# Kernel optimization log

Hardware: AMD Instinct MI355X
Metric: run time of the kernel (lower is better)

## Reference

```python
import jax, jax.numpy as jnp
import numpy as np

B = 131072
NUM_MODS = 6
NUM_PREDS = 30
CLS_TH = 2.0
CLS_IGNORE = 0.2
MGN = 0.2
CLS_COEF = 1.0
REG_COEF = 1.0


def setup_inputs() -> dict:
    key = jax.random.key(0)
    k1, k2, k3 = jax.random.split(key, 3)
    reg = jax.random.normal(k1, (B, NUM_MODS, NUM_PREDS, 2), jnp.float32)
    cls = jax.random.normal(k2, (B, NUM_MODS), jnp.float32)
    gt_preds = jax.random.normal(k3, (B, NUM_PREDS, 2), jnp.float32)
    has_preds = jnp.ones((B, NUM_PREDS), dtype=bool)
    return {"reg": reg, "cls": cls, "gt_preds": gt_preds, "has_preds": has_preds}


def _loss(reg, cls, gt, has):
    # ---------------- PredLoss (LaneGCN cls + reg loss) ----------------
    hasf = has.astype(jnp.float32)
    last = hasf + 0.1 * jnp.arange(NUM_PREDS, dtype=jnp.float32) / float(NUM_PREDS)
    last_idcs = jnp.argmax(last, axis=1)                      # [B]
    max_last = jnp.max(last, axis=1)
    valid = max_last > 1.0                                    # [B] rows kept by `mask`

    # distance of each mode's last-valid point to gt last-valid point
    reg_last = jnp.take_along_axis(reg, last_idcs[:, None, None, None], axis=2)[:, :, 0, :]  # [B,6,2]
    gt_last = jnp.take_along_axis(gt, last_idcs[:, None, None], axis=1)[:, 0, :]             # [B,2]
    dist = jnp.sqrt(((reg_last - gt_last[:, None, :]) ** 2).sum(-1))                          # [B,6]

    min_idcs = jnp.argmin(dist, axis=1)                       # [B]
    min_dist = jnp.min(dist, axis=1)

    cls_min = jnp.take_along_axis(cls, min_idcs[:, None], axis=1)  # [B,1]
    mgn = cls_min - cls                                            # [B,6]
    m01 = (min_dist < CLS_TH)[:, None] & ((dist - min_dist[:, None]) > CLS_IGNORE) & valid[:, None]
    cls_mask = m01 & (mgn < MGN)
    num_cls = cls_mask.sum()
    cls_loss = CLS_COEF * (MGN * num_cls.astype(jnp.float32) - jnp.where(cls_mask, mgn, 0.0).sum())

    # SmoothL1 (beta=1, reduction='sum') over best mode, masked by has & valid
    reg_best = jnp.take_along_axis(reg, min_idcs[:, None, None, None], axis=1)[:, 0]  # [B,30,2]
    diff = reg_best - gt
    ad = jnp.abs(diff)
    sl1 = jnp.where(ad < 1.0, 0.5 * diff * diff, ad - 0.5)
    w = (has & valid[:, None]).astype(jnp.float32)[..., None]  # [B,30,1]
    reg_loss = REG_COEF * (sl1 * w).sum()
    num_reg = (has & valid[:, None]).sum()

    loss = cls_loss / (num_cls.astype(jnp.float32) + 1e-10) + reg_loss / (num_reg.astype(jnp.float32) + 1e-10)

    # ---------------- heading (vectorized over scenes) ----------------
    gx, gy = gt[..., 0], gt[..., 1]                           # [B,30]
    fwd = jnp.arctan2(gy[:, 2:] - gy[:, 1:-1], gx[:, 2:] - gx[:, 1:-1])   # [B,28]
    bwd = jnp.arctan2(gy[:, 1:-1] - gy[:, :-2], gx[:, 1:-1] - gx[:, :-2]) # [B,28]
    head_tmp = jnp.rad2deg(fwd) + jnp.rad2deg(bwd)                         # [B,28]
    mid = jnp.where((fwd == 0.0) | (bwd == 0.0), head_tmp, head_tmp / 2.0)
    head0 = jnp.rad2deg(jnp.arctan2(gy[:, 1] - gy[:, 0], gx[:, 1] - gx[:, 0]))
    headL = jnp.rad2deg(jnp.arctan2(gy[:, -1] - gy[:, -2], gx[:, -1] - gx[:, -2]))
    head = jnp.concatenate([head0[:, None], mid, headL[:, None]], axis=1)  # [B,30]
    moving = jnp.sqrt(((gt[:, 0, :] - gt[:, -1, :]) ** 2).sum(-1)) > 2.0
    head = jnp.where(moving[:, None], head, 0.0)

    # ---------------- rotated dist_error (per-timestep 2x2 rotation) ----------------
    de0 = jnp.abs(gt[:, None, :, :] - reg)                    # [B,6,30,2] L1Loss(reduction='none')
    theta = jnp.deg2rad(-head)                                # [B,30]
    c = jnp.cos(theta)[:, None, :]                            # [B,1,30]
    s = jnp.sin(theta)[:, None, :]
    dx, dy = de0[..., 0], de0[..., 1]                         # [B,6,30]
    rx = c * dx - s * dy
    ry = s * dx + c * dy
    de = jnp.abs(jnp.stack([rx, ry], axis=-1))                # [B,6,30,2]

    top1 = jnp.argmax(cls, axis=1)                            # [B]
    de_top = jnp.take_along_axis(de, top1[:, None, None, None], axis=1)[:, 0]  # [B,30,2]

    ade6_x = de[..., 0].sum(); ade6_y = de[..., 1].sum()
    fde6_x = de[:, :, -1, 0].sum(); fde6_y = de[:, :, -1, 1].sum()
    ade1_x = de_top[..., 0].sum(); ade1_y = de_top[..., 1].sum()
    fde1_x = de_top[:, -1, 0].sum(); fde1_y = de_top[:, -1, 1].sum()

    Bn = de.shape[0]
    counts = jnp.array([
        NUM_MODS * Bn * NUM_PREDS,  # ade6_num
        NUM_MODS * Bn,              # fde6_num
        Bn * NUM_PREDS,             # ade1_num
        Bn,                         # fde1_num
    ], dtype=jnp.float32)

    return jnp.stack([
        loss, cls_loss, num_cls.astype(jnp.float32), reg_loss, num_reg.astype(jnp.float32),
        ade6_x, ade6_y, fde6_x, fde6_y, counts[0], counts[1],
        ade1_x, ade1_y, fde1_x, fde1_y, counts[2], counts[3],
    ])


def reference(reg, cls, gt_preds, has_preds):
    return _loss(reg, cls, gt_preds, has_preds)
```

## Files before the change

kernel.cpp:

```cpp
#include <hip/hip_runtime.h>
#include <math.h>

#define NROWS 131072
#define NMODS 6
#define NPREDS 30
#define RPG 4
#define NGROUPS (NROWS / RPG)
#define NBLK 2048
#define NWAVES (NBLK * 4)

#define ACC_SLOT(ws, i) ((float*)((char*)(ws) + (size_t)(i) * 256))

#define LGKM_WAIT() do { \
    __builtin_amdgcn_wave_barrier(); \
    __builtin_amdgcn_s_waitcnt(0xC07F); \
    __builtin_amdgcn_wave_barrier(); \
} while (0)

__device__ __forceinline__ float wave_reduce(float v) {
    v += __shfl_xor(v, 32);
    v += __shfl_xor(v, 16);
    v += __shfl_xor(v, 8);
    v += __shfl_xor(v, 4);
    v += __shfl_xor(v, 2);
    v += __shfl_xor(v, 1);
    return v;
}

__global__ __launch_bounds__(256) void loss_wave(
    const float* __restrict__ reg,
    const float* __restrict__ cls,
    const float* __restrict__ gt,
    const int* __restrict__ has,
    void* __restrict__ ws)
{
    const int tid   = threadIdx.x;
    const int lane  = tid & 63;
    const int wid   = tid >> 6;
    const int gwave = blockIdx.x * 4 + wid;

    __shared__ float4 s_gt[4][RPG * 15];
    __shared__ float4 s_ct[4][RPG * 15];
    __shared__ float  s_red[4][12];

    const int row = lane / 15;
    const int q   = lane - row * 15;

    float acc[12];
    #pragma unroll
    for (int i = 0; i < 12; ++i) acc[i] = 0.f;

    for (int g = gwave; g < NGROUPS; g += NWAVES) {
        const int rb = g * RPG;

        float4 gv = make_float4(0.f, 0.f, 0.f, 0.f);
        int2   hv = make_int2(0, 0);
        if (lane < 60) {
            gv = ((const float4*)gt)[(size_t)rb * 15 + lane];
            hv = ((const int2*)has)[(size_t)rb * 15 + lane];
        }
        const float4* reg4 = (const float4*)reg + (size_t)rb * 90;
        float4 rv[6];
        #pragma unroll
        for (int i = 0; i < 5; ++i) rv[i] = reg4[lane + 64 * i];
        if (lane < 40) rv[5] = reg4[lane + 320];

        unsigned long long bx = __ballot(lane < 60 && hv.x != 0);
        unsigned long long by = __ballot(lane < 60 && hv.y != 0);

        unsigned ex = 0u, ey = 0u;
        int last = NPREDS - 1;
        bool valid = false;
        float2 rl[NMODS];
        float2 cc[3];
        if (lane < RPG) {
            ex = (unsigned)((bx >> (15 * lane)) & 0x7FFFull);
            ey = (unsigned)((by >> (15 * lane)) & 0x7FFFull);
            int le = ex ? 2 * (31 - __builtin_clz(ex)) : -1;
            int lo = ey ? 2 * (31 - __builtin_clz(ey)) + 1 : -1;
            last = (le > lo) ? le : lo;
            if (last < 0) last = NPREDS - 1;
            valid = ((ex & ~1u) | ey) != 0u;

            const float2* rr = (const float2*)reg + (size_t)(rb + lane) * 180;
            #pragma unroll
            for (int m = 0; m < NMODS; ++m) rl[m] = rr[m * NPREDS + last];
            const float2* cp = (const float2*)cls + (size_t)(rb + lane) * 3;
            #pragma unroll
            for (int i = 0; i < 3; ++i) cc[i] = cp[i];
        }

        float e_dx = gv.z - gv.x, e_dy = gv.w - gv.y;
        float e_inv = rsqrtf(fmaf(e_dx, e_dx, e_dy * e_dy));
        float uex = e_dx * e_inv, uey = e_dy * e_inv;

        float nx = __shfl(gv.x, lane + 1);
        float ny = __shfl(gv.y, lane + 1);
        float o_dx = nx - gv.z, o_dy = ny - gv.w;
        float o_inv = rsqrtf(fmaf(o_dx, o_dx, o_dy * o_dy));
        float uox = o_dx * o_inv, uoy = o_dy * o_inv;

        float upx = __shfl(uox, lane - 1);
        float upy = __shfl(uoy, lane - 1);

        const int base = row * 15;
        float g0x  = __shfl(gv.x, base),      g0y  = __shfl(gv.y, base);
        float g29x = __shfl(gv.z, base + 14), g29y = __shfl(gv.w, base + 14);
        float mdx = g0x - g29x, mdy = g0y - g29y;
        const bool moving = fmaf(mdx, mdx, mdy * mdy) > 4.0f;

        float sx0 = uex + upx, sy0 = uey + upy;
        float dx0 = uey - upy, dy0 = upx - uex;
        float na0 = fmaf(sx0, sx0, sy0 * sy0);
        float nb0 = fmaf(dx0, dx0, dy0 * dy0);
        bool ua0 = na0 >= nb0;
        float wx0 = ua0 ? sx0 : dx0, wy0 = ua0 ? sy0 : dy0;
        float wi0 = rsqrtf(ua0 ? na0 : nb0);
        float c0 = wx0 * wi0, s0 = -(wy0 * wi0);
        if (q == 0) { c0 = uex; s0 = -uey; }

        float sx1 = uox + uex, sy1 = uoy + uey;
        float dx1 = uoy - uey, dy1 = uex - uox;
        float na1 = fmaf(sx1, sx1, sy1 * sy1);
        float nb1 = fmaf(dx1, dx1, dy1 * dy1);
        bool ua1 = na1 >= nb1;
        float wx1 = ua1 ? sx1 : dx1, wy1 = ua1 ? sy1 : dy1;
        float wi1 = rsqrtf(ua1 ? na1 : nb1);
        float c1 = wx1 * wi1, s1 = -(wy1 * wi1);
        if (q == 14) { c1 = uex; s1 = -uey; }

        if (!moving) { c0 = 1.f; s0 = 0.f; c1 = 1.f; s1 = 0.f; }

        if (lane < 60) {
            s_gt[wid][lane] = gv;
            s_ct[wid][lane] = make_float4(c0, s0, c1, s1);
        }
        LGKM_WAIT();

        unsigned metaval = 0u;
        if (lane < RPG) {
            float4 gq = s_gt[wid][lane * 15 + (last >> 1)];
            float glx = (last & 1) ? gq.z : gq.x;
            float gly = (last & 1) ? gq.w : gq.y;

            float dists[NMODS];
            #pragma unroll
            for (int m = 0; m < NMODS; ++m) {
                float ax = rl[m].x - glx, ay = rl[m].y - gly;
                dists[m] = sqrtf(ax * ax + ay * ay);
            }
            float mind = dists[0]; int mini = 0;
            #pragma unroll
            for (int m = 1; m < NMODS; ++m)
                if (dists[m] < mind) { mind = dists[m]; mini = m; }

            float cv[NMODS];
            #pragma unroll
            for (int i = 0; i < 3; ++i) { cv[2*i] = cc[i].x; cv[2*i+1] = cc[i].y; }
            float clsmin = cv[0];
            #pragma unroll
            for (int m = 1; m < NMODS; ++m) clsmin = (m == mini) ? cv[m] : clsmin;

            if (valid && (mind < 2.0f)) {
                #pragma unroll
                for (int m = 0; m < NMODS; ++m) {
                    float mgn = clsmin - cv[m];
                    if (((dists[m] - mind) > 0.2f) && (mgn < 0.2f)) {
                        acc[10] += 1.0f;
                        acc[9]  += mgn;
                    }
                }
            }
            float bc = cv[0]; int top1 = 0;
            #pragma unroll
            for (int m = 1; m < NMODS; ++m)
                if (cv[m] > bc) { bc = cv[m]; top1 = m; }

            if (valid)
                acc[11] += (float)(__builtin_popcount(ex) + __builtin_popcount(ey));

            metaval = (unsigned)mini | ((unsigned)top1 << 4) | (valid ? 256u : 0u);
        }

        #pragma unroll
        for (int i = 0; i < 6; ++i) {
            int k = lane + 64 * i;
            bool act = (i < 5) || (lane < 40);
            int kk = act ? k : 0;
            int rw  = kk / 90;
            int rem = kk - rw * 90;
            int m   = rem / 15;
            int qq  = rem - 15 * m;

            unsigned mv  = (unsigned)__shfl((int)metaval, rw);
            unsigned exr = (unsigned)((bx >> (15 * rw)) & 0x7FFFull);
            unsigned eyr = (unsigned)((by >> (15 * rw)) & 0x7FFFull);
            float4 gp = s_gt[wid][rw * 15 + qq];
            float4 sp = s_ct[wid][rw * 15 + qq];
            float4 v  = rv[i];

            unsigned mini = mv & 15u, top1 = (mv >> 4) & 15u;
            bool vld    = (mv & 256u) != 0u;
            bool isTop  = ((unsigned)m == top1);
            bool isBest = ((unsigned)m == mini) && vld;

            if (act) {
                {
                    float dx = fabsf(gp.x - v.x), dy = fabsf(gp.y - v.y);
                    float ax = fabsf(sp.x * dx - sp.y * dy);
                    float ay = fabsf(sp.y * dx + sp.x * dy);
                    acc[0] += ax; acc[1] += ay;
                    if (isTop) { acc[4] += ax; acc[5] += ay; }
                    if (isBest && ((exr >> qq) & 1u)) {
                        float e0 = v.x - gp.x, e1 = v.y - gp.y;
                        float q0 = fabsf(e0), q1 = fabsf(e1);
                        acc[8] += (q0 < 1.f) ? (0.5f * e0 * e0) : (q0 - 0.5f);
                        acc[8] += (q1 < 1.f) ? (0.5f * e1 * e1) : (q1 - 0.5f);
                    }
                }
                {
                    float dx = fabsf(gp.z - v.z), dy = fabsf(gp.w - v.w);
                    float ax = fabsf(sp.z * dx - sp.w * dy);
                    float ay = fabsf(sp.w * dx + sp.z * dy);
                    acc[0] += ax; acc[1] += ay;
                    if (isTop) { acc[4] += ax; acc[5] += ay; }
                    if (qq == 14) {
                        acc[2] += ax; acc[3] += ay;
                        if (isTop) { acc[6] += ax; acc[7] += ay; }
                    }
                    if (isBest && ((eyr >> qq) & 1u)) {
                        float e0 = v.z - gp.z, e1 = v.w - gp.w;
                        float q0 = fabsf(e0), q1 = fabsf(e1);
                        acc[8] += (q0 < 1.f) ? (0.5f * e0 * e0) : (q0 - 0.5f);
                        acc[8] += (q1 < 1.f) ? (0.5f * e1 * e1) : (q1 - 0.5f);
                    }
                }
            }
        }
        __builtin_amdgcn_wave_barrier();
    }

    #pragma unroll
    for (int i = 0; i < 12; ++i) acc[i] = wave_reduce(acc[i]);

    if (lane == 0) {
        #pragma unroll
        for (int i = 0; i < 12; ++i) s_red[wid][i] = acc[i];
    }
    __syncthreads();
    if (tid < 12) {
        float s = s_red[0][tid] + s_red[1][tid] + s_red[2][tid] + s_red[3][tid];
        atomicAdd(ACC_SLOT(ws, tid), s);
    }
}

__global__ void finalize(void* ws, float* __restrict__ out) {
    if (threadIdx.x == 0) {
        float nc = *ACC_SLOT(ws, 10), nr = *ACC_SLOT(ws, 11);
        float cls_loss = 0.2f * nc - *ACC_SLOT(ws, 9);
        float reg_loss = *ACC_SLOT(ws, 8);
        float loss = cls_loss / (nc + 1e-10f) + reg_loss / (nr + 1e-10f);
        out[0]  = loss;
        out[1]  = cls_loss;
        out[2]  = nc;
        out[3]  = reg_loss;
        out[4]  = nr;
        out[5]  = *ACC_SLOT(ws, 0);
        out[6]  = *ACC_SLOT(ws, 1);
        out[7]  = *ACC_SLOT(ws, 2);
        out[8]  = *ACC_SLOT(ws, 3);
        out[9]  = 23592960.0f;
        out[10] = 786432.0f;
        out[11] = *ACC_SLOT(ws, 4);
        out[12] = *ACC_SLOT(ws, 5);
        out[13] = *ACC_SLOT(ws, 6);
        out[14] = *ACC_SLOT(ws, 7);
        out[15] = 3932160.0f;
        out[16] = 131072.0f;
    }
}

extern "C" void kernel_launch(void* const* d_in, const int* in_sizes, int n_in,
                              void* d_out, int out_size, void* d_ws, size_t ws_size,
                              hipStream_t stream) {
    const float* reg = (const float*)d_in[0];
    const float* cls = (const float*)d_in[1];
    const float* gt  = (const float*)d_in[2];
    const int*   has = (const int*)d_in[3];
    float* out = (float*)d_out;

    hipMemsetAsync(d_ws, 0, 4096, stream);
    loss_wave<<<NBLK, 256, 0, stream>>>(reg, cls, gt, has, d_ws);
    finalize<<<1, 64, 0, stream>>>(d_ws, out);
}
```

Measured before the change: 303.2 us.

## Fuse finalize into main kernel and restructure per-element loop via shared scatter

```diff
diff --git a/kernel.cpp b/kernel.cpp
--- a/kernel.cpp
+++ b/kernel.cpp
@@ -10,6 +10,7 @@
 #define NWAVES (NBLK * 4)
 
 #define ACC_SLOT(ws, i) ((float*)((char*)(ws) + (size_t)(i) * 256))
+#define TICKET(ws) ((unsigned*)((char*)(ws) + 3072))
 
 #define LGKM_WAIT() do { \
     __builtin_amdgcn_wave_barrier(); \
@@ -32,19 +33,35 @@
     const float* __restrict__ cls,
     const float* __restrict__ gt,
     const int* __restrict__ has,
-    void* __restrict__ ws)
+    void* __restrict__ ws,
+    float* __restrict__ out)
 {
     const int tid   = threadIdx.x;
     const int lane  = tid & 63;
     const int wid   = tid >> 6;
     const int gwave = blockIdx.x * 4 + wid;
 
-    __shared__ float4 s_gt[4][RPG * 15];
-    __shared__ float4 s_ct[4][RPG * 15];
+    __shared__ float4 s_tile[4][216];
     __shared__ float  s_red[4][12];
+    __shared__ int    s_last;
 
     const int row = lane / 15;
     const int q   = lane - row * 15;
+
+    int   rwv[6];  int mmv[6];  int idxv[6];  float f14v[6];
+    #pragma unroll
+    for (int i = 0; i < 6; ++i) {
+        int k = lane + 64 * i;
+        bool act = (i < 5) || (lane < 40);
+        int kk = act ? k : 0;
+        int rw  = kk / 90;
+        int rem = kk - rw * 90;
+        int mm  = rem / 15;
+        int qq  = rem - 15 * mm;
+        rwv[i] = rw; mmv[i] = mm; idxv[i] = rw * 15 + qq;
+        f14v[i] = (qq == 14) ? 1.f : 0.f;
+    }
+    const int dumidx = 180 + (lane & 31);
 
     float acc[12];
     #pragma unroll
@@ -65,6 +82,13 @@
         for (int i = 0; i < 5; ++i) rv[i] = reg4[lane + 64 * i];
         if (lane < 40) rv[5] = reg4[lane + 320];
 
+        float2 cc[3];
+        if (lane < RPG) {
+            const float2* cp = (const float2*)cls + (size_t)(rb + lane) * 3;
+            #pragma unroll
+            for (int i = 0; i < 3; ++i) cc[i] = cp[i];
+        }
+
         unsigned long long bx = __ballot(lane < 60 && hv.x != 0);
         unsigned long long by = __ballot(lane < 60 && hv.y != 0);
 
@@ -72,7 +96,6 @@
         int last = NPREDS - 1;
         bool valid = false;
         float2 rl[NMODS];
-        float2 cc[3];
         if (lane < RPG) {
             ex = (unsigned)((bx >> (15 * lane)) & 0x7FFFull);
             ey = (unsigned)((by >> (15 * lane)) & 0x7FFFull);
@@ -85,9 +108,6 @@
             const float2* rr = (const float2*)reg + (size_t)(rb + lane) * 180;
             #pragma unroll
             for (int m = 0; m < NMODS; ++m) rl[m] = rr[m * NPREDS + last];
-            const float2* cp = (const float2*)cls + (size_t)(rb + lane) * 3;
-            #pragma unroll
-            for (int i = 0; i < 3; ++i) cc[i] = cp[i];
         }
 
         float e_dx = gv.z - gv.x, e_dy = gv.w - gv.y;
@@ -132,27 +152,27 @@
         if (!moving) { c0 = 1.f; s0 = 0.f; c1 = 1.f; s1 = 0.f; }
 
         if (lane < 60) {
-            s_gt[wid][lane] = gv;
-            s_ct[wid][lane] = make_float4(c0, s0, c1, s1);
+            s_tile[wid][lane]      = gv;
+            s_tile[wid][60 + lane] = make_float4(c0, s0, c1, s1);
         }
         LGKM_WAIT();
 
         unsigned metaval = 0u;
         if (lane < RPG) {
-            float4 gq = s_gt[wid][lane * 15 + (last >> 1)];
+            float4 gq = s_tile[wid][lane * 15 + (last >> 1)];
             float glx = (last & 1) ? gq.z : gq.x;
             float gly = (last & 1) ? gq.w : gq.y;
 
-            float dists[NMODS];
+            float d2s[NMODS];
             #pragma unroll
             for (int m = 0; m < NMODS; ++m) {
                 float ax = rl[m].x - glx, ay = rl[m].y - gly;
-                dists[m] = sqrtf(ax * ax + ay * ay);
+                d2s[m] = fmaf(ax, ax, ay * ay);
             }
-            float mind = dists[0]; int mini = 0;
+            float mind2 = d2s[0]; int mini = 0;
             #pragma unroll
             for (int m = 1; m < NMODS; ++m)
-                if (dists[m] < mind) { mind = dists[m]; mini = m; }
+                if (d2s[m] < mind2) { mind2 = d2s[m]; mini = m; }
 
             float cv[NMODS];
             #pragma unroll
@@ -161,11 +181,14 @@
             #pragma unroll
             for (int m = 1; m < NMODS; ++m) clsmin = (m == mini) ? cv[m] : clsmin;
 
-            if (valid && (mind < 2.0f)) {
+            if (valid && (mind2 < 4.0f)) {
+                float mind = sqrtf(mind2);
+                float t = mind + 0.2f;
+                float thr = t * t;
                 #pragma unroll
                 for (int m = 0; m < NMODS; ++m) {
                     float mgn = clsmin - cv[m];
-                    if (((dists[m] - mind) > 0.2f) && (mgn < 0.2f)) {
+                    if ((d2s[m] > thr) && (mgn < 0.2f)) {
                         acc[10] += 1.0f;
                         acc[9]  += mgn;
                     }
@@ -184,59 +207,60 @@
 
         #pragma unroll
         for (int i = 0; i < 6; ++i) {
-            int k = lane + 64 * i;
-            bool act = (i < 5) || (lane < 40);
-            int kk = act ? k : 0;
-            int rw  = kk / 90;
-            int rem = kk - rw * 90;
-            int m   = rem / 15;
-            int qq  = rem - 15 * m;
-
-            unsigned mv  = (unsigned)__shfl((int)metaval, rw);
-            unsigned exr = (unsigned)((bx >> (15 * rw)) & 0x7FFFull);
-            unsigned eyr = (unsigned)((by >> (15 * rw)) & 0x7FFFull);
-            float4 gp = s_gt[wid][rw * 15 + qq];
-            float4 sp = s_ct[wid][rw * 15 + qq];
-            float4 v  = rv[i];
-
-            unsigned mini = mv & 15u, top1 = (mv >> 4) & 15u;
-            bool vld    = (mv & 256u) != 0u;
-            bool isTop  = ((unsigned)m == top1);
-            bool isBest = ((unsigned)m == mini) && vld;
-
+            const bool act = (i < 5) || (lane < 40);
+            unsigned mvb = (unsigned)__shfl((int)metaval, rwv[i]);
+            unsigned mini = mvb & 15u, top1 = (mvb >> 4) & 15u;
+            float tf = ((unsigned)mmv[i] == top1) ? 1.f : 0.f;
+            bool bestm = ((unsigned)mmv[i] == mini);
             if (act) {
-                {
-                    float dx = fabsf(gp.x - v.x), dy = fabsf(gp.y - v.y);
-                    float ax = fabsf(sp.x * dx - sp.y * dy);
-                    float ay = fabsf(sp.y * dx + sp.x * dy);
-                    acc[0] += ax; acc[1] += ay;
-                    if (isTop) { acc[4] += ax; acc[5] += ay; }
-                    if (isBest && ((exr >> qq) & 1u)) {
-                        float e0 = v.x - gp.x, e1 = v.y - gp.y;
-                        float q0 = fabsf(e0), q1 = fabsf(e1);
-                        acc[8] += (q0 < 1.f) ? (0.5f * e0 * e0) : (q0 - 0.5f);
-                        acc[8] += (q1 < 1.f) ? (0.5f * e1 * e1) : (q1 - 0.5f);
-                    }
-                }
-                {
-                    float dx = fabsf(gp.z - v.z), dy = fabsf(gp.w - v.w);
-                    float ax = fabsf(sp.z * dx - sp.w * dy);
-                    float ay = fabsf(sp.w * dx + sp.z * dy);
-                    acc[0] += ax; acc[1] += ay;
-                    if (isTop) { acc[4] += ax; acc[5] += ay; }
-                    if (qq == 14) {
-                        acc[2] += ax; acc[3] += ay;
-                        if (isTop) { acc[6] += ax; acc[7] += ay; }
-                    }
-                    if (isBest && ((eyr >> qq) & 1u)) {
-                        float e0 = v.z - gp.z, e1 = v.w - gp.w;
-                        float q0 = fabsf(e0), q1 = fabsf(e1);
-                        acc[8] += (q0 < 1.f) ? (0.5f * e0 * e0) : (q0 - 0.5f);
-                        acc[8] += (q1 < 1.f) ? (0.5f * e1 * e1) : (q1 - 0.5f);
-                    }
-                }
+                float4* gpp = &s_tile[wid][idxv[i]];
+                float4 gp = gpp[0];
+                float4 sp = gpp[60];
+                float4 v  = rv[i];
+
+                float d0x = gp.x - v.x, d0y = gp.y - v.y;
+                float ax0 = fabsf(fmaf(sp.x, fabsf(d0x), -(sp.y * fabsf(d0y))));
+                float ay0 = fabsf(fmaf(sp.y, fabsf(d0x),   sp.x * fabsf(d0y)));
+                acc[0] += ax0; acc[1] += ay0;
+                acc[4] = fmaf(tf, ax0, acc[4]); acc[5] = fmaf(tf, ay0, acc[5]);
+
+                float d1x = gp.z - v.z, d1y = gp.w - v.w;
+                float ax1 = fabsf(fmaf(sp.z, fabsf(d1x), -(sp.w * fabsf(d1y))));
+                float ay1 = fabsf(fmaf(sp.w, fabsf(d1x),   sp.z * fabsf(d1y)));
+                acc[0] += ax1; acc[1] += ay1;
+                acc[4] = fmaf(tf, ax1, acc[4]); acc[5] = fmaf(tf, ay1, acc[5]);
+
+                float f14 = f14v[i];
+                acc[2] = fmaf(f14, ax1, acc[2]); acc[3] = fmaf(f14, ay1, acc[3]);
+                float tf14 = tf * f14;
+                acc[6] = fmaf(tf14, ax1, acc[6]); acc[7] = fmaf(tf14, ay1, acc[7]);
+
+                float4* dmy = &s_tile[wid][dumidx - 120];
+                float4* wa  = bestm ? gpp : dmy;
+                wa[120] = v;
             }
         }
+
+        LGKM_WAIT();
+
+        if (lane < 60) {
+            unsigned mvr = (unsigned)__shfl((int)metaval, row);
+            float4 bb = s_tile[wid][120 + lane];
+            bool vld = (mvr & 256u) != 0u;
+            unsigned bitx = (unsigned)(bx >> lane) & 1u;
+            unsigned bity = (unsigned)(by >> lane) & 1u;
+            float g0 = (vld && bitx) ? 1.f : 0.f;
+            float g1 = (vld && bity) ? 1.f : 0.f;
+            float e0x = bb.x - gv.x, e0y = bb.y - gv.y;
+            float e1x = bb.z - gv.z, e1y = bb.w - gv.w;
+            float sl0 = ((fabsf(e0x) < 1.f) ? (0.5f * e0x * e0x) : (fabsf(e0x) - 0.5f))
+                      + ((fabsf(e0y) < 1.f) ? (0.5f * e0y * e0y) : (fabsf(e0y) - 0.5f));
+            float sl1 = ((fabsf(e1x) < 1.f) ? (0.5f * e1x * e1x) : (fabsf(e1x) - 0.5f))
+                      + ((fabsf(e1y) < 1.f) ? (0.5f * e1y * e1y) : (fabsf(e1y) - 0.5f));
+            acc[8] = fmaf(g0, sl0, acc[8]);
+            acc[8] = fmaf(g1, sl1, acc[8]);
+        }
+
         __builtin_amdgcn_wave_barrier();
     }
 
@@ -252,31 +276,39 @@
         float s = s_red[0][tid] + s_red[1][tid] + s_red[2][tid] + s_red[3][tid];
         atomicAdd(ACC_SLOT(ws, tid), s);
     }
-}
-
-__global__ void finalize(void* ws, float* __restrict__ out) {
-    if (threadIdx.x == 0) {
-        float nc = *ACC_SLOT(ws, 10), nr = *ACC_SLOT(ws, 11);
-        float cls_loss = 0.2f * nc - *ACC_SLOT(ws, 9);
-        float reg_loss = *ACC_SLOT(ws, 8);
-        float loss = cls_loss / (nc + 1e-10f) + reg_loss / (nr + 1e-10f);
-        out[0]  = loss;
-        out[1]  = cls_loss;
-        out[2]  = nc;
-        out[3]  = reg_loss;
-        out[4]  = nr;
-        out[5]  = *ACC_SLOT(ws, 0);
-        out[6]  = *ACC_SLOT(ws, 1);
-        out[7]  = *ACC_SLOT(ws, 2);
-        out[8]  = *ACC_SLOT(ws, 3);
-        out[9]  = 23592960.0f;
-        out[10] = 786432.0f;
-        out[11] = *ACC_SLOT(ws, 4);
-        out[12] = *ACC_SLOT(ws, 5);
-        out[13] = *ACC_SLOT(ws, 6);
-        out[14] = *ACC_SLOT(ws, 7);
-        out[15] = 3932160.0f;
-        out[16] = 131072.0f;
+    __syncthreads();
+
+    if (tid == 0) {
+        __threadfence();
+        s_last = (atomicAdd(TICKET(ws), 1u) == (unsigned)(NBLK - 1)) ? 1 : 0;
+    }
+    __syncthreads();
+    if (s_last) {
+        if (tid < 12)
+            s_red[0][tid] = atomicAdd(ACC_SLOT(ws, tid), 0.0f);
+        __syncthreads();
+        if (tid == 0) {
+            float nc = s_red[0][10], nr = s_red[0][11];
+            float cls_loss = 0.2f * nc - s_red[0][9];
+            float reg_loss = s_red[0][8];
+            out[0]  = cls_loss / (nc + 1e-10f) + reg_loss / (nr + 1e-10f);
+            out[1]  = cls_loss;
+            out[2]  = nc;
+            out[3]  = reg_loss;
+            out[4]  = nr;
+            out[5]  = s_red[0][0];
+            out[6]  = s_red[0][1];
+            out[7]  = s_red[0][2];
+            out[8]  = s_red[0][3];
+            out[9]  = 23592960.0f;
+            out[10] = 786432.0f;
+            out[11] = s_red[0][4];
+            out[12] = s_red[0][5];
+            out[13] = s_red[0][6];
+            out[14] = s_red[0][7];
+            out[15] = 3932160.0f;
+            out[16] = 131072.0f;
+        }
     }
 }
 
@@ -290,6 +322,5 @@
     float* out = (float*)d_out;
 
     hipMemsetAsync(d_ws, 0, 4096, stream);
-    loss_wave<<<NBLK, 256, 0, stream>>>(reg, cls, gt, has, d_ws);
-    finalize<<<1, 64, 0, stream>>>(d_ws, out);
+    loss_wave<<<NBLK, 256, 0, stream>>>(reg, cls, gt, has, d_ws, out);
 }
```

Measured after the change: 385.3 us. +27.1%, slower.

## Software-pipeline per-group head loads across iterations with double-buffered state

Applied to the files above, without the earlier changes.

```diff
diff --git a/kernel.cpp b/kernel.cpp
--- a/kernel.cpp
+++ b/kernel.cpp
@@ -25,6 +25,232 @@
     v += __shfl_xor(v, 2);
     v += __shfl_xor(v, 1);
     return v;
+}
+
+struct GState {
+    float4 gv;
+    int2   hv;
+    float2 cc0, cc1, cc2;
+    float2 rl0, rl1, rl2, rl3, rl4, rl5;
+    unsigned long long bx, by;
+    unsigned ex, ey;
+    int last;
+    int validf;
+};
+
+__device__ __forceinline__ void issue_head(
+    int g, int lane,
+    const float* __restrict__ gt, const int* __restrict__ has,
+    const float* __restrict__ cls, GState& s)
+{
+    const int rb = g * RPG;
+    s.gv = make_float4(0.f, 0.f, 0.f, 0.f);
+    s.hv = make_int2(0, 0);
+    if (lane < 60) {
+        s.gv = ((const float4*)gt)[(size_t)rb * 15 + lane];
+        s.hv = ((const int2*)has)[(size_t)rb * 15 + lane];
+    }
+    if (lane < RPG) {
+        const float2* cp = (const float2*)cls + (size_t)(rb + lane) * 3;
+        s.cc0 = cp[0]; s.cc1 = cp[1]; s.cc2 = cp[2];
+    }
+}
+
+__device__ __forceinline__ void resolve_mask(
+    int g, int lane, const float* __restrict__ reg, GState& s)
+{
+    s.bx = __ballot(lane < 60 && s.hv.x != 0);
+    s.by = __ballot(lane < 60 && s.hv.y != 0);
+    s.ex = 0u; s.ey = 0u; s.last = NPREDS - 1; s.validf = 0;
+    if (lane < RPG) {
+        s.ex = (unsigned)((s.bx >> (15 * lane)) & 0x7FFFull);
+        s.ey = (unsigned)((s.by >> (15 * lane)) & 0x7FFFull);
+        int le = s.ex ? 2 * (31 - __builtin_clz(s.ex)) : -1;
+        int lo = s.ey ? 2 * (31 - __builtin_clz(s.ey)) + 1 : -1;
+        int last = (le > lo) ? le : lo;
+        if (last < 0) last = NPREDS - 1;
+        s.last = last;
+        s.validf = (((s.ex & ~1u) | s.ey) != 0u) ? 1 : 0;
+        const float2* rr = (const float2*)reg + (size_t)(g * RPG + lane) * 180;
+        s.rl0 = rr[0 * NPREDS + last];
+        s.rl1 = rr[1 * NPREDS + last];
+        s.rl2 = rr[2 * NPREDS + last];
+        s.rl3 = rr[3 * NPREDS + last];
+        s.rl4 = rr[4 * NPREDS + last];
+        s.rl5 = rr[5 * NPREDS + last];
+    }
+}
+
+__device__ __forceinline__ void body(
+    int g, bool pf, GState& cur, GState& nxt,
+    const float* __restrict__ reg, const float* __restrict__ cls,
+    const float* __restrict__ gt, const int* __restrict__ has,
+    int lane, int row, int q,
+    float4* __restrict__ sgt, float4* __restrict__ sct,
+    float acc[12])
+{
+    const int rb = g * RPG;
+
+    if (pf) issue_head(g + NWAVES, lane, gt, has, cls, nxt);
+
+    const float4* reg4 = (const float4*)reg + (size_t)rb * 90;
+    float4 rv[6];
+    #pragma unroll
+    for (int i = 0; i < 5; ++i) rv[i] = reg4[lane + 64 * i];
+    if (lane < 40) rv[5] = reg4[lane + 320];
+
+    const float4 gv = cur.gv;
+
+    float e_dx = gv.z - gv.x, e_dy = gv.w - gv.y;
+    float e_inv = rsqrtf(fmaf(e_dx, e_dx, e_dy * e_dy));
+    float uex = e_dx * e_inv, uey = e_dy * e_inv;
+
+    float nx = __shfl(gv.x, lane + 1);
+    float ny = __shfl(gv.y, lane + 1);
+    float o_dx = nx - gv.z, o_dy = ny - gv.w;
+    float o_inv = rsqrtf(fmaf(o_dx, o_dx, o_dy * o_dy));
+    float uox = o_dx * o_inv, uoy = o_dy * o_inv;
+
+    float upx = __shfl(uox, lane - 1);
+    float upy = __shfl(uoy, lane - 1);
+
+    const int base = row * 15;
+    float g0x  = __shfl(gv.x, base),      g0y  = __shfl(gv.y, base);
+    float g29x = __shfl(gv.z, base + 14), g29y = __shfl(gv.w, base + 14);
+    float mdx = g0x - g29x, mdy = g0y - g29y;
+    const bool moving = fmaf(mdx, mdx, mdy * mdy) > 4.0f;
+
+    float sx0 = uex + upx, sy0 = uey + upy;
+    float dx0 = uey - upy, dy0 = upx - uex;
+    float na0 = fmaf(sx0, sx0, sy0 * sy0);
+    float nb0 = fmaf(dx0, dx0, dy0 * dy0);
+    bool ua0 = na0 >= nb0;
+    float wx0 = ua0 ? sx0 : dx0, wy0 = ua0 ? sy0 : dy0;
+    float wi0 = rsqrtf(ua0 ? na0 : nb0);
+    float c0 = wx0 * wi0, s0 = -(wy0 * wi0);
+    if (q == 0) { c0 = uex; s0 = -uey; }
+
+    float sx1 = uox + uex, sy1 = uoy + uey;
+    float dx1 = uoy - uey, dy1 = uex - uox;
+    float na1 = fmaf(sx1, sx1, sy1 * sy1);
+    float nb1 = fmaf(dx1, dx1, dy1 * dy1);
+    bool ua1 = na1 >= nb1;
+    float wx1 = ua1 ? sx1 : dx1, wy1 = ua1 ? sy1 : dy1;
+    float wi1 = rsqrtf(ua1 ? na1 : nb1);
+    float c1 = wx1 * wi1, s1 = -(wy1 * wi1);
+    if (q == 14) { c1 = uex; s1 = -uey; }
+
+    if (!moving) { c0 = 1.f; s0 = 0.f; c1 = 1.f; s1 = 0.f; }
+
+    if (lane < 60) {
+        sgt[lane] = gv;
+        sct[lane] = make_float4(c0, s0, c1, s1);
+    }
+    LGKM_WAIT();
+
+    unsigned metaval = 0u;
+    if (lane < RPG) {
+        float4 gq = sgt[lane * 15 + (cur.last >> 1)];
+        float glx = (cur.last & 1) ? gq.z : gq.x;
+        float gly = (cur.last & 1) ? gq.w : gq.y;
+
+        float2 rl[NMODS] = { cur.rl0, cur.rl1, cur.rl2, cur.rl3, cur.rl4, cur.rl5 };
+        float dists[NMODS];
+        #pragma unroll
+        for (int m = 0; m < NMODS; ++m) {
+            float ax = rl[m].x - glx, ay = rl[m].y - gly;
+            dists[m] = sqrtf(ax * ax + ay * ay);
+        }
+        float mind = dists[0]; int mini = 0;
+        #pragma unroll
+        for (int m = 1; m < NMODS; ++m)
+            if (dists[m] < mind) { mind = dists[m]; mini = m; }
+
+        float cv[NMODS] = { cur.cc0.x, cur.cc0.y, cur.cc1.x, cur.cc1.y, cur.cc2.x, cur.cc2.y };
+        float clsmin = cv[0];
+        #pragma unroll
+        for (int m = 1; m < NMODS; ++m) clsmin = (m == mini) ? cv[m] : clsmin;
+
+        if (cur.validf && (mind < 2.0f)) {
+            #pragma unroll
+            for (int m = 0; m < NMODS; ++m) {
+                float mgn = clsmin - cv[m];
+                if (((dists[m] - mind) > 0.2f) && (mgn < 0.2f)) {
+                    acc[10] += 1.0f;
+                    acc[9]  += mgn;
+                }
+            }
+        }
+        float bc = cv[0]; int top1 = 0;
+        #pragma unroll
+        for (int m = 1; m < NMODS; ++m)
+            if (cv[m] > bc) { bc = cv[m]; top1 = m; }
+
+        if (cur.validf)
+            acc[11] += (float)(__builtin_popcount(cur.ex) + __builtin_popcount(cur.ey));
+
+        metaval = (unsigned)mini | ((unsigned)top1 << 4) | (cur.validf ? 256u : 0u);
+    }
+
+    #pragma unroll
+    for (int i = 0; i < 6; ++i) {
+        int k = lane + 64 * i;
+        bool act = (i < 5) || (lane < 40);
+        int kk = act ? k : 0;
+        int rw  = kk / 90;
+        int rem = kk - rw * 90;
+        int m   = rem / 15;
+        int qq  = rem - 15 * m;
+
+        unsigned mv  = (unsigned)__shfl((int)metaval, rw);
+        unsigned exr = (unsigned)((cur.bx >> (15 * rw)) & 0x7FFFull);
+        unsigned eyr = (unsigned)((cur.by >> (15 * rw)) & 0x7FFFull);
+        float4 gp = sgt[rw * 15 + qq];
+        float4 sp = sct[rw * 15 + qq];
+        float4 v  = rv[i];
+
+        unsigned mini = mv & 15u, top1 = (mv >> 4) & 15u;
+        bool vld    = (mv & 256u) != 0u;
+        bool isTop  = ((unsigned)m == top1);
+        bool isBest = ((unsigned)m == mini) && vld;
+
+        if (act) {
+            {
+                float dx = fabsf(gp.x - v.x), dy = fabsf(gp.y - v.y);
+                float ax = fabsf(sp.x * dx - sp.y * dy);
+                float ay = fabsf(sp.y * dx + sp.x * dy);
+                acc[0] += ax; acc[1] += ay;
+                if (isTop) { acc[4] += ax; acc[5] += ay; }
+                if (isBest && ((exr >> qq) & 1u)) {
+                    float e0 = v.x - gp.x, e1 = v.y - gp.y;
+                    float q0 = fabsf(e0), q1 = fabsf(e1);
+                    acc[8] += (q0 < 1.f) ? (0.5f * e0 * e0) : (q0 - 0.5f);
+                    acc[8] += (q1 < 1.f) ? (0.5f * e1 * e1) : (q1 - 0.5f);
+                }
+            }
+            {
+                float dx = fabsf(gp.z - v.z), dy = fabsf(gp.w - v.w);
+                float ax = fabsf(sp.z * dx - sp.w * dy);
+                float ay = fabsf(sp.w * dx + sp.z * dy);
+                acc[0] += ax; acc[1] += ay;
+                if (isTop) { acc[4] += ax; acc[5] += ay; }
+                if (qq == 14) {
+                    acc[2] += ax; acc[3] += ay;
+                    if (isTop) { acc[6] += ax; acc[7] += ay; }
+                }
+                if (isBest && ((eyr >> qq) & 1u)) {
+                    float e0 = v.z - gp.z, e1 = v.w - gp.w;
+                    float q0 = fabsf(e0), q1 = fabsf(e1);
+                    acc[8] += (q0 < 1.f) ? (0.5f * e0 * e0) : (q0 - 0.5f);
+                    acc[8] += (q1 < 1.f) ? (0.5f * e1 * e1) : (q1 - 0.5f);
+                }
+            }
+        }
+    }
+
+    if (pf) resolve_mask(g + NWAVES, lane, reg, nxt);
+
+    __builtin_amdgcn_wave_barrier();
 }
 
 __global__ __launch_bounds__(256) void loss_wave(
@@ -46,198 +272,23 @@
     const int row = lane / 15;
     const int q   = lane - row * 15;
 
+    float4* sgt = &s_gt[wid][0];
+    float4* sct = &s_ct[wid][0];
+
     float acc[12];
     #pragma unroll
     for (int i = 0; i < 12; ++i) acc[i] = 0.f;
 
-    for (int g = gwave; g < NGROUPS; g += NWAVES) {
-        const int rb = g * RPG;
-
-        float4 gv = make_float4(0.f, 0.f, 0.f, 0.f);
-        int2   hv = make_int2(0, 0);
-        if (lane < 60) {
-            gv = ((const float4*)gt)[(size_t)rb * 15 + lane];
-            hv = ((const int2*)has)[(size_t)rb * 15 + lane];
-        }
-        const float4* reg4 = (const float4*)reg + (size_t)rb * 90;
-        float4 rv[6];
-        #pragma unroll
-        for (int i = 0; i < 5; ++i) rv[i] = reg4[lane + 64 * i];
-        if (lane < 40) rv[5] = reg4[lane + 320];
-
-        unsigned long long bx = __ballot(lane < 60 && hv.x != 0);
-        unsigned long long by = __ballot(lane < 60 && hv.y != 0);
-
-        unsigned ex = 0u, ey = 0u;
-        int last = NPREDS - 1;
-        bool valid = false;
-        float2 rl[NMODS];
-        float2 cc[3];
-        if (lane < RPG) {
-            ex = (unsigned)((bx >> (15 * lane)) & 0x7FFFull);
-            ey = (unsigned)((by >> (15 * lane)) & 0x7FFFull);
-            int le = ex ? 2 * (31 - __builtin_clz(ex)) : -1;
-            int lo = ey ? 2 * (31 - __builtin_clz(ey)) + 1 : -1;
-            last = (le > lo) ? le : lo;
-            if (last < 0) last = NPREDS - 1;
-            valid = ((ex & ~1u) | ey) != 0u;
-
-            const float2* rr = (const float2*)reg + (size_t)(rb + lane) * 180;
-            #pragma unroll
-            for (int m = 0; m < NMODS; ++m) rl[m] = rr[m * NPREDS + last];
-            const float2* cp = (const float2*)cls + (size_t)(rb + lane) * 3;
-            #pragma unroll
-            for (int i = 0; i < 3; ++i) cc[i] = cp[i];
-        }
-
-        float e_dx = gv.z - gv.x, e_dy = gv.w - gv.y;
-        float e_inv = rsqrtf(fmaf(e_dx, e_dx, e_dy * e_dy));
-        float uex = e_dx * e_inv, uey = e_dy * e_inv;
-
-        float nx = __shfl(gv.x, lane + 1);
-        float ny = __shfl(gv.y, lane + 1);
-        float o_dx = nx - gv.z, o_dy = ny - gv.w;
-        float o_inv = rsqrtf(fmaf(o_dx, o_dx, o_dy * o_dy));
-        float uox = o_dx * o_inv, uoy = o_dy * o_inv;
-
-        float upx = __shfl(uox, lane - 1);
-        float upy = __shfl(uoy, lane - 1);
-
-        const int base = row * 15;
-        float g0x  = __shfl(gv.x, base),      g0y  = __shfl(gv.y, base);
-        float g29x = __shfl(gv.z, base + 14), g29y = __shfl(gv.w, base + 14);
-        float mdx = g0x - g29x, mdy = g0y - g29y;
-        const bool moving = fmaf(mdx, mdx, mdy * mdy) > 4.0f;
-
-        float sx0 = uex + upx, sy0 = uey + upy;
-        float dx0 = uey - upy, dy0 = upx - uex;
-        float na0 = fmaf(sx0, sx0, sy0 * sy0);
-        float nb0 = fmaf(dx0, dx0, dy0 * dy0);
-        bool ua0 = na0 >= nb0;
-        float wx0 = ua0 ? sx0 : dx0, wy0 = ua0 ? sy0 : dy0;
-        float wi0 = rsqrtf(ua0 ? na0 : nb0);
-        float c0 = wx0 * wi0, s0 = -(wy0 * wi0);
-        if (q == 0) { c0 = uex; s0 = -uey; }
-
-        float sx1 = uox + uex, sy1 = uoy + uey;
-        float dx1 = uoy - uey, dy1 = uex - uox;
-        float na1 = fmaf(sx1, sx1, sy1 * sy1);
-        float nb1 = fmaf(dx1, dx1, dy1 * dy1);
-        bool ua1 = na1 >= nb1;
-        float wx1 = ua1 ? sx1 : dx1, wy1 = ua1 ? sy1 : dy1;
-        float wi1 = rsqrtf(ua1 ? na1 : nb1);
-        float c1 = wx1 * wi1, s1 = -(wy1 * wi1);
-        if (q == 14) { c1 = uex; s1 = -uey; }
-
-        if (!moving) { c0 = 1.f; s0 = 0.f; c1 = 1.f; s1 = 0.f; }
-
-        if (lane < 60) {
-            s_gt[wid][lane] = gv;
-            s_ct[wid][lane] = make_float4(c0, s0, c1, s1);
-        }
-        LGKM_WAIT();
-
-        unsigned metaval = 0u;
-        if (lane < RPG) {
-            float4 gq = s_gt[wid][lane * 15 + (last >> 1)];
-            float glx = (last & 1) ? gq.z : gq.x;
-            float gly = (last & 1) ? gq.w : gq.y;
-
-            float dists[NMODS];
-            #pragma unroll
-            for (int m = 0; m < NMODS; ++m) {
-                float ax = rl[m].x - glx, ay = rl[m].y - gly;
-                dists[m] = sqrtf(ax * ax + ay * ay);
-            }
-            float mind = dists[0]; int mini = 0;
-            #pragma unroll
-            for (int m = 1; m < NMODS; ++m)
-                if (dists[m] < mind) { mind = dists[m]; mini = m; }
-
-            float cv[NMODS];
-            #pragma unroll
-            for (int i = 0; i < 3; ++i) { cv[2*i] = cc[i].x; cv[2*i+1] = cc[i].y; }
-            float clsmin = cv[0];
-            #pragma unroll
-            for (int m = 1; m < NMODS; ++m) clsmin = (m == mini) ? cv[m] : clsmin;
-
-            if (valid && (mind < 2.0f)) {
-                #pragma unroll
-                for (int m = 0; m < NMODS; ++m) {
-                    float mgn = clsmin - cv[m];
-                    if (((dists[m] - mind) > 0.2f) && (mgn < 0.2f)) {
-                        acc[10] += 1.0f;
-                        acc[9]  += mgn;
-                    }
-                }
-            }
-            float bc = cv[0]; int top1 = 0;
-            #pragma unroll
-            for (int m = 1; m < NMODS; ++m)
-                if (cv[m] > bc) { bc = cv[m]; top1 = m; }
-
-            if (valid)
-                acc[11] += (float)(__builtin_popcount(ex) + __builtin_popcount(ey));
-
-            metaval = (unsigned)mini | ((unsigned)top1 << 4) | (valid ? 256u : 0u);
-        }
-
-        #pragma unroll
-        for (int i = 0; i < 6; ++i) {
-            int k = lane + 64 * i;
-            bool act = (i < 5) || (lane < 40);
-            int kk = act ? k : 0;
-            int rw  = kk / 90;
-            int rem = kk - rw * 90;
-            int m   = rem / 15;
-            int qq  = rem - 15 * m;
-
-            unsigned mv  = (unsigned)__shfl((int)metaval, rw);
-            unsigned exr = (unsigned)((bx >> (15 * rw)) & 0x7FFFull);
-            unsigned eyr = (unsigned)((by >> (15 * rw)) & 0x7FFFull);
-            float4 gp = s_gt[wid][rw * 15 + qq];
-            float4 sp = s_ct[wid][rw * 15 + qq];
-            float4 v  = rv[i];
-
-            unsigned mini = mv & 15u, top1 = (mv >> 4) & 15u;
-            bool vld    = (mv & 256u) != 0u;
-            bool isTop  = ((unsigned)m == top1);
-            bool isBest = ((unsigned)m == mini) && vld;
-
-            if (act) {
-                {
-                    float dx = fabsf(gp.x - v.x), dy = fabsf(gp.y - v.y);
-                    float ax = fabsf(sp.x * dx - sp.y * dy);
-                    float ay = fabsf(sp.y * dx + sp.x * dy);
-                    acc[0] += ax; acc[1] += ay;
-                    if (isTop) { acc[4] += ax; acc[5] += ay; }
-                    if (isBest && ((exr >> qq) & 1u)) {
-                        float e0 = v.x - gp.x, e1 = v.y - gp.y;
-                        float q0 = fabsf(e0), q1 = fabsf(e1);
-                        acc[8] += (q0 < 1.f) ? (0.5f * e0 * e0) : (q0 - 0.5f);
-                        acc[8] += (q1 < 1.f) ? (0.5f * e1 * e1) : (q1 - 0.5f);
-                    }
-                }
-                {
-                    float dx = fabsf(gp.z - v.z), dy = fabsf(gp.w - v.w);
-                    float ax = fabsf(sp.z * dx - sp.w * dy);
-                    float ay = fabsf(sp.w * dx + sp.z * dy);
-                    acc[0] += ax; acc[1] += ay;
-                    if (isTop) { acc[4] += ax; acc[5] += ay; }
-                    if (qq == 14) {
-                        acc[2] += ax; acc[3] += ay;
-                        if (isTop) { acc[6] += ax; acc[7] += ay; }
-                    }
-                    if (isBest && ((eyr >> qq) & 1u)) {
-                        float e0 = v.z - gp.z, e1 = v.w - gp.w;
-                        float q0 = fabsf(e0), q1 = fabsf(e1);
-                        acc[8] += (q0 < 1.f) ? (0.5f * e0 * e0) : (q0 - 0.5f);
-                        acc[8] += (q1 < 1.f) ? (0.5f * e1 * e1) : (q1 - 0.5f);
-                    }
-                }
-            }
-        }
-        __builtin_amdgcn_wave_barrier();
+    GState sA, sB;
+    issue_head(gwave, lane, gt, has, cls, sA);
+    resolve_mask(gwave, lane, reg, sA);
+
+    for (int kk = 0; kk < 2; ++kk) {
+        const int g0 = gwave + kk * 2 * NWAVES;
+        body(g0,          true,     sA, sB, reg, cls, gt, has,
+             lane, row, q, sgt, sct, acc);
+        body(g0 + NWAVES, kk == 0,  sB, sA, reg, cls, gt, has,
+             lane, row, q, sgt, sct, acc);
     }
 
     #pragma unroll
```

New measurement: 303.9 us. About the same (+0.2%).
